# Optimization experiments

Hardware: AMD Instinct MI355X
Metric: run time of the kernel (lower is better)

## Reference

```python
import jax, jax.numpy as jnp
import numpy as np
from jax import lax

H, W = 480, 320
BS, PAD, SF, WIN = 20, 6, 4, 32        # block, zero-pad, scale, window = BS+2*PAD
NH, NW = H // BS, W // BS              # 24, 16 -> 384 blocks


def _conv(x, w, b, stride=1, pad=0):
    out = lax.conv_general_dilated(x, w, (stride, stride), [(pad, pad), (pad, pad)],
                                   dimension_numbers=('NCHW', 'OIHW', 'NCHW'))
    return out + b[None, :, None, None]


def _rep_conv(x, w, b):  # 3x3 conv with replicate padding (padding_mode='replicate')
    xp = jnp.pad(x, ((0, 0), (0, 0), (1, 1), (1, 1)), mode='edge')
    return _conv(xp, w, b)


def _maxpool2(x):
    return lax.reduce_window(x, -jnp.inf, lax.max, (1, 1, 2, 2), (1, 1, 2, 2), 'VALID')


def _pixel_shuffle(x, r=SF):  # (N, C*r*r, h, w) -> (N, C, h*r, w*r), torch ordering
    n, crr, h, w = x.shape
    c = crr // (r * r)
    return x.reshape(n, c, r, r, h, w).transpose(0, 1, 4, 2, 5, 3).reshape(n, c, h * r, w * r)


def _he(key, shape):
    std = np.sqrt(2.0 / (shape[0] * shape[2] * shape[3]))
    return jax.random.normal(key, shape, jnp.float32) * std


def setup_inputs() -> dict:
    key = jax.random.key(0)
    ks = jax.random.split(key, 16)
    return {
        'x': jax.random.normal(ks[0], (1, 3, H, W), jnp.float32),
        'cls_w1': _he(ks[1], (32, 3, 3, 3)),  'cls_b1': jnp.zeros((32,), jnp.float32),
        'cls_w2': _he(ks[2], (32, 32, 3, 3)), 'cls_b2': jnp.zeros((32,), jnp.float32),
        'cls_w3': _he(ks[3], (16, 32, 3, 3)), 'cls_b3': jnp.zeros((16,), jnp.float32),
        'cls_w4': _he(ks[4], (8, 16, 3, 3)),  'cls_b4': jnp.zeros((8,), jnp.float32),
        'cls_w5': _he(ks[5], (1, 8, 5, 5)),   'cls_b5': jnp.zeros((1,), jnp.float32),
        'lt_w1': _he(ks[6], (16, 3, 3, 3)),   'lt_b1': jnp.zeros((16,), jnp.float32),
        'lt_w2': _he(ks[7], (48, 16, 3, 3)),  'lt_b2': jnp.zeros((48,), jnp.float32),
        'cx_w1': _he(ks[8], (64, 3, 3, 3)),   'cx_b1': jnp.zeros((64,), jnp.float32),
        'cx_w2': _he(ks[9], (64, 64, 3, 3)),  'cx_b2': jnp.zeros((64,), jnp.float32),
        'cx_w3': _he(ks[10], (48, 64, 3, 3)), 'cx_b3': jnp.zeros((48,), jnp.float32),
    }


def reference(x, cls_w1, cls_b1, cls_w2, cls_b2, cls_w3, cls_b3, cls_w4, cls_b4,
              cls_w5, cls_b5, lt_w1, lt_b1, lt_w2, lt_b2,
              cx_w1, cx_b1, cx_w2, cx_b2, cx_w3, cx_b3):
    relu = jax.nn.relu
    # ---- classifier (gate) ----
    h = relu(_rep_conv(x, cls_w1, cls_b1))
    h = _maxpool2(relu(_rep_conv(h, cls_w2, cls_b2)))
    h = relu(_rep_conv(h, cls_w3, cls_b3))
    h = _maxpool2(relu(_rep_conv(h, cls_w4, cls_b4)))
    h = _conv(h, cls_w5, cls_b5, stride=BS // 4)          # (1,1,NH,NW)
    class_vector = jax.nn.sigmoid(h.reshape(-1))          # (NH*NW,)

    # ---- blockify (overlapping 32x32 windows, stride 20, zero pad 6) ----
    xp = jnp.pad(x, ((0, 0), (0, 0), (PAD, PAD), (PAD, PAD)))
    hidx = jnp.arange(NH)[:, None] * BS + jnp.arange(WIN)
    widx = jnp.arange(NW)[:, None] * BS + jnp.arange(WIN)
    t = xp[:, :, hidx]
    t = t[:, :, :, :, widx]
    blocks = t.transpose(0, 2, 4, 1, 3, 5).reshape(NH * NW, 3, WIN, WIN)

    # ---- experts (run on all blocks; mask-select == one-hot gather/scatter) ----
    lt = _pixel_shuffle(_conv(relu(_conv(blocks, lt_w1, lt_b1, pad=1)), lt_w2, lt_b2, pad=1))
    lt = jnp.clip(lt, 0.0, 1.0)
    cx = relu(_conv(blocks, cx_w1, cx_b1, pad=1))
    cx = relu(_conv(cx, cx_w2, cx_b2, pad=1))
    cx = jnp.clip(_pixel_shuffle(_conv(cx, cx_w3, cx_b3, pad=1)), 0.0, 1.0)

    is_complex = class_vector > 0.5
    out = jnp.where(is_complex[:, None, None, None], cx, lt)  # (N,3,128,128)

    # ---- crop halo and reassemble full image ----
    c0 = SF * PAD
    out = out[:, :, c0:c0 + SF * BS, c0:c0 + SF * BS]          # (N,3,80,80)
    img = out.reshape(NH, NW, 3, SF * BS, SF * BS)
    img = img.transpose(2, 0, 3, 1, 4).reshape(1, 3, NH * SF * BS, NW * SF * BS)
    return img, class_vector
```

## Files before the change

### kernel.cpp

```cpp
#include <hip/hip_runtime.h>
#include <hip/hip_bf16.h>
#include <math.h>

static constexpr int H = 480, W = 320, NH = 24, NW = 16, NB = 384;
static constexpr int HW = H * W;
static constexpr int H2 = 240, W2 = 160;
static constexpr int HW2 = H2 * W2;
static constexpr int H4 = 120, W4 = 80;
static constexpr int HW4 = H4 * W4;
static constexpr int IMG_PIX = 3 * 1920 * 1280;

typedef __attribute__((ext_vector_type(8))) short short8;
typedef __attribute__((ext_vector_type(4))) float f32x4;
typedef __attribute__((ext_vector_type(8))) unsigned short ushort8;

static constexpr int WQ_CX2 = 0;
static constexpr int WQ_CX3 = 36864;
static constexpr int WQ_LT2 = 64512;
static constexpr int WQ_FCX = 78336;
static constexpr int WQ_FLT = 80384;
static constexpr int WQ_CLS2 = 80896;
static constexpr int WPK_ALL = 108544;

__device__ __forceinline__ int iclamp(int v, int lo, int hi) {
    return v < lo ? lo : (v > hi ? hi : v);
}
__device__ __forceinline__ unsigned short f2bfu(float x) {
    __hip_bfloat16 h = __float2bfloat16(x);
    return *reinterpret_cast<unsigned short*>(&h);
}
__device__ __forceinline__ float bf2f(unsigned short u) {
    __hip_bfloat16 h = *reinterpret_cast<__hip_bfloat16*>(&u);
    return __bfloat162float(h);
}

__global__ __launch_bounds__(256) void k_prep(const float* __restrict__ x,
                                              const float* __restrict__ cls_w1,
                                              const float* __restrict__ cls_b1,
                                              const float* __restrict__ cx_w2,
                                              const float* __restrict__ cx_w3,
                                              const float* __restrict__ lt_w2,
                                              const float* __restrict__ cx_w1,
                                              const float* __restrict__ lt_w1,
                                              const float* __restrict__ cls_w2,
                                              unsigned short* __restrict__ c1s,
                                              unsigned short* __restrict__ wpk) {
    int blk = blockIdx.x;
    if (blk < 600) {
        int p = blk * 256 + threadIdx.x;
        int y = p / W, xx = p - y * W;
        float in[27];
#pragma unroll
        for (int ci = 0; ci < 3; ++ci)
#pragma unroll
            for (int dy = 0; dy < 3; ++dy) {
                int yy = iclamp(y + dy - 1, 0, H - 1);
#pragma unroll
                for (int dx = 0; dx < 3; ++dx) {
                    int xc = iclamp(xx + dx - 1, 0, W - 1);
                    in[ci * 9 + dy * 3 + dx] = x[ci * HW + yy * W + xc];
                }
            }
#pragma unroll
        for (int coc = 0; coc < 4; ++coc) {
            ushort8 hv, mv, lv;
#pragma unroll
            for (int c8 = 0; c8 < 8; ++c8) {
                int co = coc * 8 + c8;
                float acc = cls_b1[co];
#pragma unroll
                for (int k = 0; k < 27; ++k) acc = fmaf(cls_w1[co * 27 + k], in[k], acc);
                float v = fmaxf(acc, 0.f);
                unsigned short h = f2bfu(v);
                float r1 = v - bf2f(h);
                unsigned short m = f2bfu(r1);
                unsigned short l = f2bfu(r1 - bf2f(m));
                hv[c8] = h; mv[c8] = m; lv[c8] = l;
            }
            *(ushort8*)(c1s + (long)p * 32 + coc * 8) = hv;
            *(ushort8*)(c1s + (long)32 * HW + (long)p * 32 + coc * 8) = mv;
            *(ushort8*)(c1s + (long)64 * HW + (long)p * 32 + coc * 8) = lv;
        }
        return;
    }
    int i = (blk - 600) * 256 + threadIdx.x;
    if (i >= WPK_ALL) return;
    float v = 0.f;
    if (i < WQ_CX3) {
        int c = i >> 9, r = i & 511;
        int lane = r >> 3, j = r & 7;
        int col = lane & 15, kq = lane >> 4;
        int nt = c & 3, kc = (c >> 2) & 1, t = c >> 3;
        int co = nt * 16 + col, ci = kc * 32 + kq * 8 + j;
        v = cx_w2[(co * 64 + ci) * 9 + t];
    } else if (i < WQ_LT2) {
        int c = (i - WQ_CX3) >> 9, r = i & 511;
        int lane = r >> 3, j = r & 7;
        int col = lane & 15, kq = lane >> 4;
        int nt = c % 3, q = c / 3;
        int kc = q & 1, t = q >> 1;
        int co = nt * 16 + col, ci = kc * 32 + kq * 8 + j;
        v = cx_w3[(co * 64 + ci) * 9 + t];
    } else if (i < WQ_FCX) {
        int c = (i - WQ_LT2) >> 9, r = i & 511;
        int lane = r >> 3, j = r & 7;
        int col = lane & 15, kq = lane >> 4;
        int nt = c % 3, t = c / 3;
        int co = nt * 16 + col, ci = kq * 8 + j;
        v = (ci < 16) ? lt_w2[(co * 16 + ci) * 9 + t] : 0.f;
    } else if (i < WQ_FLT) {
        int c = (i - WQ_FCX) >> 9, r = i & 511;
        int lane = r >> 3, j = r & 7;
        int col = lane & 15, kq = lane >> 4;
        int co = c * 16 + col, k = kq * 8 + j;
        v = (k < 27) ? cx_w1[co * 27 + k] : 0.f;
    } else if (i < WQ_CLS2) {
        int r = i & 511;
        int lane = r >> 3, j = r & 7;
        int col = lane & 15, kq = lane >> 4;
        int k = kq * 8 + j;
        v = (k < 27) ? lt_w1[col * 27 + k] : 0.f;
    } else {
        int c = (i - WQ_CLS2) >> 9, r = i & 511;
        int lane = r >> 3, j = r & 7;
        int col = lane & 15, kq = lane >> 4;
        int nt = c & 1, q = c >> 1;
        int t = q % 9, pl = q / 9;
        int co = nt * 16 + col, ci = kq * 8 + j;
        float w = cls_w2[(co * 32 + ci) * 9 + t];
        unsigned short h = f2bfu(w);
        float r1 = w - bf2f(h);
        unsigned short m = f2bfu(r1);
        unsigned short l = f2bfu(r1 - bf2f(m));
        wpk[i] = pl == 0 ? h : (pl == 1 ? m : l);
        return;
    }
    wpk[i] = f2bfu(v);
}


template <int P>
__device__ __forceinline__ void cls2_phase(const unsigned short* __restrict__ src,
                                           unsigned short* __restrict__ sh2,
                                           const unsigned short* __restrict__ wb,
                                           f32x4 acc[4][2], int tid, int ty, int tx) {
    int lane = tid & 63, wave = tid >> 6;
    int col = lane & 15, kq = lane >> 4;
    __syncthreads();
    for (int idx = tid; idx < 1296; idx += 256) {
        int pix = idx >> 2, g = idx & 3;
        int hy = iclamp(ty * 16 + pix / 18 - 1, 0, H - 1);
        int hx = iclamp(tx * 16 + pix % 18 - 1, 0, W - 1);
        ushort8 v = *(const ushort8*)(src + ((long)(hy * W + hx)) * 32 + g * 8);
        *(ushort8*)(sh2 + pix * 32 + ((g ^ ((pix >> 1) & 3)) * 8)) = v;
    }
    __syncthreads();
#pragma unroll
    for (int t = 0; t < 9; ++t) {
        int dy = t / 3, dx = t - dy * 3;
        short8 B[2][P];
#pragma unroll
        for (int nt = 0; nt < 2; ++nt)
#pragma unroll
            for (int pl = 0; pl < P; ++pl)
                B[nt][pl] = *(const short8*)(wb + ((pl * 9 + t) * 2 + nt) * 512 + lane * 8);
#pragma unroll
        for (int i = 0; i < 4; ++i) {
            int pix = (wave * 4 + i + dy) * 18 + col + dx;
            short8 a = *(const short8*)(sh2 + pix * 32 + ((kq ^ ((pix >> 1) & 3)) * 8));
#pragma unroll
            for (int nt = 0; nt < 2; ++nt)
#pragma unroll
                for (int pl = 0; pl < P; ++pl)
                    acc[i][nt] = __builtin_amdgcn_mfma_f32_16x16x32_bf16(a, B[nt][pl],
                                                                         acc[i][nt], 0, 0, 0);
        }
    }
}

__global__ __launch_bounds__(256, 2) void k_cls2m(const unsigned short* __restrict__ c1s,
                                                  const unsigned short* __restrict__ wpk,
                                                  const float* __restrict__ b2,
                                                  float* __restrict__ c2) {
    extern __shared__ unsigned short sh2[];
    int tid = threadIdx.x;
    int tile = blockIdx.x;
    int ty = tile / 20, tx = tile - ty * 20;
    int lane = tid & 63, wave = tid >> 6;
    int col = lane & 15, kq = lane >> 4;
    const unsigned short* wb = wpk + WQ_CLS2;
    f32x4 acc[4][2];
#pragma unroll
    for (int nt = 0; nt < 2; ++nt) {
        float bv = b2[nt * 16 + col];
#pragma unroll
        for (int i = 0; i < 4; ++i) acc[i][nt] = f32x4{bv, bv, bv, bv};
    }
    cls2_phase<3>(c1s, sh2, wb, acc, tid, ty, tx);
    cls2_phase<2>(c1s + (long)32 * HW, sh2, wb + 18 * 512, acc, tid, ty, tx);
    cls2_phase<1>(c1s + (long)64 * HW, sh2, wb + 36 * 512, acc, tid, ty, tx);
    __syncthreads();
    float* pool = (float*)sh2;
#pragma unroll
    for (int i = 0; i < 4; ++i)
#pragma unroll
        for (int nt = 0; nt < 2; ++nt)
#pragma unroll
            for (int rr = 0; rr < 4; ++rr)
                pool[(nt * 16 + col) * 257 + (wave * 4 + i) * 16 + kq * 4 + rr] =
                    fmaxf(acc[i][nt][rr], 0.f);
    __syncthreads();
#pragma unroll
    for (int k = 0; k < 8; ++k) {
        int o = tid + k * 256;
        int co = o >> 6, rem = o & 63;
        int py = rem >> 3, px = rem & 7;
        const float* lp = pool + co * 257 + py * 32 + px * 2;
        float m = fmaxf(fmaxf(lp[0], lp[1]), fmaxf(lp[16], lp[17]));
        c2[co * HW2 + (ty * 8 + py) * W2 + tx * 8 + px] = m;
    }
}

__global__ __launch_bounds__(256) void k_cls3(const float* __restrict__ in,
                                              const float* __restrict__ w,
                                              const float* __restrict__ b,
                                              float* __restrict__ p3) {
    int p = blockIdx.x * 256 + threadIdx.x;
    if (p >= HW2) return;
    int cc = blockIdx.y;
    int s = blockIdx.z;
    int y = p / W2, xx = p - y * W2;
    float acc[8];
#pragma unroll
    for (int co = 0; co < 8; ++co) acc[co] = s ? 0.f : b[cc * 8 + co];
    for (int cil = 0; cil < 16; ++cil) {
        int ci = s * 16 + cil;
        float v[9];
#pragma unroll
        for (int dy = 0; dy < 3; ++dy) {
            int yy = iclamp(y + dy - 1, 0, H2 - 1);
#pragma unroll
            for (int dx = 0; dx < 3; ++dx) {
                int xc = iclamp(xx + dx - 1, 0, W2 - 1);
                v[dy * 3 + dx] = in[ci * HW2 + yy * W2 + xc];
            }
        }
#pragma unroll
        for (int co = 0; co < 8; ++co)
#pragma unroll
            for (int k = 0; k < 9; ++k)
                acc[co] = fmaf(w[(cc * 8 + co) * 288 + ci * 9 + k], v[k], acc[co]);
    }
#pragma unroll
    for (int co = 0; co < 8; ++co) p3[(s * 16 + cc * 8 + co) * HW2 + p] = acc[co];
}

__global__ __launch_bounds__(256) void k_cls4f(const float* __restrict__ p3,
                                               const float* __restrict__ w,
                                               const float* __restrict__ b,
                                               float* __restrict__ out) {
    __shared__ float lds[8 * 256];
    int t = threadIdx.x;
    int tile = blockIdx.x;
    int ty = tile / 10, tx = tile - ty * 10;
    int ly = t >> 4, lx = t & 15;
    int y = ty * 16 + ly, xx = tx * 16 + lx;
    float acc[8];
#pragma unroll
    for (int co = 0; co < 8; ++co) acc[co] = b[co];
    for (int ci = 0; ci < 16; ++ci) {
        float v[9];
#pragma unroll
        for (int dy = 0; dy < 3; ++dy) {
            int yy = iclamp(y + dy - 1, 0, H2 - 1);
#pragma unroll
            for (int dx = 0; dx < 3; ++dx) {
                int xc = iclamp(xx + dx - 1, 0, W2 - 1);
                int idx = ci * HW2 + yy * W2 + xc;
                v[dy * 3 + dx] = fmaxf(p3[idx] + p3[idx + 16 * HW2], 0.f);
            }
        }
#pragma unroll
        for (int co = 0; co < 8; ++co) {
            const float* wp = w + co * 144 + ci * 9;
#pragma unroll
            for (int k = 0; k < 9; ++k) acc[co] = fmaf(wp[k], v[k], acc[co]);
        }
    }
#pragma unroll
    for (int co = 0; co < 8; ++co) lds[co * 256 + t] = fmaxf(acc[co], 0.f);
    __syncthreads();
#pragma unroll
    for (int k = 0; k < 2; ++k) {
        int o = t + k * 256;
        int co = o >> 6, rem = o & 63;
        int py = rem >> 3, px = rem & 7;
        const float* lp = lds + co * 256 + py * 32 + px * 2;
        float m = fmaxf(fmaxf(lp[0], lp[1]), fmaxf(lp[16], lp[17]));
        out[co * HW4 + (ty * 8 + py) * W4 + tx * 8 + px] = m;
    }
}

__global__ __launch_bounds__(64) void k_cls5(const float* __restrict__ in,
                                             const float* __restrict__ w,
                                             const float* __restrict__ b,
                                             float* __restrict__ clsv,
                                             float* __restrict__ out_cls) {
    int bidx = blockIdx.x;
    int oy = bidx / NW, ox = bidx - oy * NW;
    int lane = threadIdx.x;
    float s = 0.f;
    for (int k = lane; k < 200; k += 64) {
        int ci = k / 25, r = k - ci * 25;
        int ky = r / 5, kx = r - ky * 5;
        s = fmaf(w[k], in[ci * HW4 + (oy * 5 + ky) * W4 + (ox * 5 + kx)], s);
    }
#pragma unroll
    for (int off = 32; off; off >>= 1) s += __shfl_down(s, off, 64);
    if (lane == 0) {
        float sig = 1.f / (1.f + expf(-(s + b[0])));
        clsv[bidx] = sig;
        out_cls[bidx] = sig;
    }
}

__global__ __launch_bounds__(512)
__attribute__((amdgpu_waves_per_eu(4, 8)))
void k_block(const float* __restrict__ x,
             const unsigned short* __restrict__ wpk,
             const float* __restrict__ lt_b1,
             const float* __restrict__ cx_b1,
             const float* __restrict__ lt_b2,
             const float* __restrict__ cx_b2,
             const float* __restrict__ cx_b3,
             const float* __restrict__ clsv,
             float* __restrict__ out) {
    extern __shared__ unsigned short sh[];
    unsigned short* T1 = sh;
    unsigned short* T2 = sh;
    unsigned short* XH = sh + 16384;
    unsigned short* WB = sh + 17408;
    int wg = blockIdx.x;
    int b = wg / 5, e = wg - b * 5;
    bool cx = clsv[b] > 0.5f;
    int bh = b / NW, bw = b - bh * NW;
    int base = 6 + 4 * e;
    int tid = threadIdx.x;
    int lane = tid & 63, wave = tid >> 6;
    int col = lane & 15, kq = lane >> 4;

    if (!cx) {
        ushort8 z = {0, 0, 0, 0, 0, 0, 0, 0};
        for (int i = tid; i < 1024; i += 512) *(ushort8*)(T1 + i * 8) = z;
    }
    if (tid < 340) {
        int xr = tid / 34, xcc = tid - xr * 34;
        int yg = bh * 20 + (base - 3 + xr) - 6;
        int xg = bw * 20 + (xcc - 1) - 6;
        bool ok = (unsigned)yg < (unsigned)H && (unsigned)xg < (unsigned)W;
#pragma unroll
        for (int ci = 0; ci < 3; ++ci)
            XH[ci * 340 + tid] = ok ? f2bfu(x[ci * HW + yg * W + xg])
                                    : (unsigned short)0;
    }
    __syncthreads();

    if (cx) {
        short8 Bf[4];
        float bv[4];
#pragma unroll
        for (int nt = 0; nt < 4; ++nt) {
            Bf[nt] = *(const short8*)(wpk + WQ_FCX + nt * 512 + lane * 8);
            bv[nt] = cx_b1[nt * 16 + col];
        }
#pragma unroll
        for (int i = 0; i < 2; ++i) {
            int mt = wave + 8 * i;
            int tr = mt >> 1, xc0 = (mt & 1) << 4;
            short8 av;
#pragma unroll
            for (int j = 0; j < 8; ++j) {
                int k = kq * 8 + j;
                int kk = k < 27 ? k : 0;
                int ci = kk / 9, t = kk - ci * 9;
                int dy = t / 3, dx = t - dy * 3;
                unsigned short v = XH[ci * 340 + (tr + dy) * 34 + (xc0 + col + dx)];
                av[j] = (k < 27) ? (short)v : (short)0;
            }
#pragma unroll
            for (int nt = 0; nt < 4; ++nt) {
                f32x4 acc = {bv[nt], bv[nt], bv[nt], bv[nt]};
                acc = __builtin_amdgcn_mfma_f32_16x16x32_bf16(av, Bf[nt], acc, 0, 0, 0);
                int co = nt * 16 + col;
#pragma unroll
                for (int r = 0; r < 4; ++r) {
                    int p1 = mt * 16 + kq * 4 + r;
                    T1[p1 * 64 + (((co >> 3) ^ (p1 & 7)) << 3) + (co & 7)] =
                        f2bfu(fmaxf(acc[r], 0.f));
                }
            }
        }
        {
            ushort8 nb0 = *(const ushort8*)(wpk + WQ_CX2 + tid * 8);
            *(ushort8*)(WB + tid * 8) = nb0;
        }
    } else {
        short8 Bf = *(const short8*)(wpk + WQ_FLT + lane * 8);
        float bv = lt_b1[col];
#pragma unroll
        for (int i = 0; i < 2; ++i) {
            int mt = wave + 8 * i;
            int tr = mt >> 1, xc0 = (mt & 1) << 4;
            short8 av;
#pragma unroll
            for (int j = 0; j < 8; ++j) {
                int k = kq * 8 + j;
                int kk = k < 27 ? k : 0;
                int ci = kk / 9, t = kk - ci * 9;
                int dy = t / 3, dx = t - dy * 3;
                unsigned short v = XH[ci * 340 + (tr + dy) * 34 + (xc0 + col + dx)];
                av[j] = (k < 27) ? (short)v : (short)0;
            }
            f32x4 acc = {bv, bv, bv, bv};
            acc = __builtin_amdgcn_mfma_f32_16x16x32_bf16(av, Bf, acc, 0, 0, 0);
#pragma unroll
            for (int r = 0; r < 4; ++r) {
                int p1 = mt * 16 + kq * 4 + r;
                T1[p1 * 32 + (((col >> 3) ^ ((p1 >> 1) & 3)) << 3) + (col & 7)] =
                    f2bfu(fmaxf(acc[r], 0.f));
            }
        }
        if (tid < 192) {
            ushort8 nb0 = *(const ushort8*)(wpk + WQ_LT2 + tid * 8);
            *(ushort8*)(WB + tid * 8) = nb0;
        }
    }
    __syncthreads();

    if (cx) {
        {
            f32x4 acc[2][4];
#pragma unroll
            for (int nt = 0; nt < 4; ++nt) {
                float bv = cx_b2[nt * 16 + col];
#pragma unroll
                for (int i = 0; i < 2; ++i) acc[i][nt] = f32x4{bv, bv, bv, bv};
            }
#pragma unroll
            for (int t = 0; t < 9; ++t) {
                int dy = t / 3, dx = t - dy * 3;
                ushort8 nb;
                if (t < 8)
                    nb = *(const ushort8*)(wpk + WQ_CX2 + (t + 1) * 4096 + tid * 8);
                const unsigned short* WBc = WB + (t & 1) * 4096;
                short8 B[4][2];
#pragma unroll
                for (int nt = 0; nt < 4; ++nt)
#pragma unroll
                    for (int kc = 0; kc < 2; ++kc)
                        B[nt][kc] = *(const short8*)(WBc + (kc * 4 + nt) * 512 + lane * 8);
#pragma unroll
                for (int i = 0; i < 2; ++i) {
                    int mt = wave + 8 * i;
                    if (mt >= 12) continue;
                    int tr = (mt >> 1) + dy;
                    int xs = ((mt & 1) << 4) + col + dx - 1;
                    bool xv = (unsigned)xs < 32u;
                    int xcl = xs < 0 ? 0 : (xs > 31 ? 31 : xs);
                    int p1 = tr * 32 + xcl;
#pragma unroll
                    for (int kc = 0; kc < 2; ++kc) {
                        int c = kc * 4 + kq;
                        short8 a = *(const short8*)(T1 + p1 * 64 + ((c ^ (p1 & 7)) << 3));
                        if (!xv) a = short8{0, 0, 0, 0, 0, 0, 0, 0};
#pragma unroll
                        for (int nt = 0; nt < 4; ++nt)
                            acc[i][nt] = __builtin_amdgcn_mfma_f32_16x16x32_bf16(
                                a, B[nt][kc], acc[i][nt], 0, 0, 0);
                    }
                }
                if (t < 8)
                    *(ushort8*)(WB + ((t + 1) & 1) * 4096 + tid * 8) = nb;
                __syncthreads();
            }
#pragma unroll
            for (int i = 0; i < 2; ++i) {
                int mt = wave + 8 * i;
                if (mt >= 12) continue;
#pragma unroll
                for (int nt = 0; nt < 4; ++nt) {
                    int co = nt * 16 + col;
#pragma unroll
                    for (int r = 0; r < 4; ++r) {
                        int p2 = mt * 16 + kq * 4 + r;
                        T2[p2 * 64 + (((co >> 3) ^ (p2 & 7)) << 3) + (co & 7)] =
                            f2bfu(fmaxf(acc[i][nt][r], 0.f));
                    }
                }
            }
            if (tid < 384) {
                ushort8 nb0 = *(const ushort8*)(wpk + WQ_CX3 + tid * 8);
                *(ushort8*)(WB + tid * 8) = nb0;
            }
        }
        __syncthreads();
        {
            int mt = wave;
            f32x4 acc[3];
#pragma unroll
            for (int nt = 0; nt < 3; ++nt) {
                float bv = cx_b3[nt * 16 + col];
                acc[nt] = f32x4{bv, bv, bv, bv};
            }
#pragma unroll
            for (int t = 0; t < 9; ++t) {
                int dy = t / 3, dx = t - dy * 3;
                ushort8 nb;
                if (t < 8 && tid < 384)
                    nb = *(const ushort8*)(wpk + WQ_CX3 + (t + 1) * 3072 + tid * 8);
                const unsigned short* WBc = WB + (t & 1) * 4096;
                short8 B[3][2];
#pragma unroll
                for (int nt = 0; nt < 3; ++nt)
#pragma unroll
                    for (int kc = 0; kc < 2; ++kc)
                        B[nt][kc] = *(const short8*)(WBc + (kc * 3 + nt) * 512 + lane * 8);
                int tr2 = (mt >> 1) + dy;
                int xs = ((mt & 1) << 4) + col + dx - 1;
                bool xv = (unsigned)xs < 32u;
                int xcl = xs < 0 ? 0 : (xs > 31 ? 31 : xs);
                int p2 = tr2 * 32 + xcl;
#pragma unroll
                for (int kc = 0; kc < 2; ++kc) {
                    int c = kc * 4 + kq;
                    short8 a = *(const short8*)(T2 + p2 * 64 + ((c ^ (p2 & 7)) << 3));
                    if (!xv) a = short8{0, 0, 0, 0, 0, 0, 0, 0};
#pragma unroll
                    for (int nt = 0; nt < 3; ++nt)
                        acc[nt] = __builtin_amdgcn_mfma_f32_16x16x32_bf16(
                            a, B[nt][kc], acc[nt], 0, 0, 0);
                }
                if (t < 8) {
                    if (tid < 384)
                        *(ushort8*)(WB + ((t + 1) & 1) * 4096 + tid * 8) = nb;
                    __syncthreads();
                }
            }
            int py = base + (mt >> 1);
#pragma unroll
            for (int nt = 0; nt < 3; ++nt) {
                int co = nt * 16 + col;
                int ch = co >> 4, dy2 = (co >> 2) & 3, dx2 = co & 3;
#pragma unroll
                for (int r = 0; r < 4; ++r) {
                    int p = mt * 16 + kq * 4 + r;
                    int px = p & 31;
                    int s0 = px * 4 + dx2 - 24;
                    if ((unsigned)s0 < 80u) {
                        int r0 = py * 4 + dy2 - 24;
                        float v = fminf(fmaxf(acc[nt][r], 0.f), 1.f);
                        out[ch * 2457600 + (bh * 80 + r0) * 1280 + bw * 80 + s0] = v;
                    }
                }
            }
        }
    } else {
        int mt = wave;
        f32x4 acc[3];
#pragma unroll
        for (int nt = 0; nt < 3; ++nt) {
            float bv = lt_b2[nt * 16 + col];
            acc[nt] = f32x4{bv, bv, bv, bv};
        }
#pragma unroll
        for (int t = 0; t < 9; ++t) {
            int dy = t / 3, dx = t - dy * 3;
            ushort8 nb;
            if (t < 8 && tid < 192)
                nb = *(const ushort8*)(wpk + WQ_LT2 + (t + 1) * 1536 + tid * 8);
            const unsigned short* WBc = WB + (t & 1) * 4096;
            short8 B[3];
#pragma unroll
            for (int nt = 0; nt < 3; ++nt)
                B[nt] = *(const short8*)(WBc + nt * 512 + lane * 8);
            int tr = (mt >> 1) + 1 + dy;
            int xs = ((mt & 1) << 4) + col + dx - 1;
            bool xv = (unsigned)xs < 32u;
            int xcl = xs < 0 ? 0 : (xs > 31 ? 31 : xs);
            int p1 = tr * 32 + xcl;
            short8 a = *(const short8*)(T1 + p1 * 32 + ((kq ^ ((p1 >> 1) & 3)) << 3));
            if (!xv) a = short8{0, 0, 0, 0, 0, 0, 0, 0};
#pragma unroll
            for (int nt = 0; nt < 3; ++nt)
                acc[nt] = __builtin_amdgcn_mfma_f32_16x16x32_bf16(a, B[nt], acc[nt], 0, 0, 0);
            if (t < 8) {
                if (tid < 192)
                    *(ushort8*)(WB + ((t + 1) & 1) * 4096 + tid * 8) = nb;
                __syncthreads();
            }
        }
        int py = base + (mt >> 1);
#pragma unroll
        for (int nt = 0; nt < 3; ++nt) {
            int co = nt * 16 + col;
            int ch = co >> 4, dy2 = (co >> 2) & 3, dx2 = co & 3;
#pragma unroll
            for (int r = 0; r < 4; ++r) {
                int p = mt * 16 + kq * 4 + r;
                int px = p & 31;
                int s0 = px * 4 + dx2 - 24;
                if ((unsigned)s0 < 80u) {
                    int r0 = py * 4 + dy2 - 24;
                    float v = fminf(fmaxf(acc[nt][r], 0.f), 1.f);
                    out[ch * 2457600 + (bh * 80 + r0) * 1280 + bw * 80 + s0] = v;
                }
            }
        }
    }
}

extern "C" void kernel_launch(void* const* d_in, const int* in_sizes, int n_in,
                              void* d_out, int out_size, void* d_ws, size_t ws_size,
                              hipStream_t stream) {
    const float* x      = (const float*)d_in[0];
    const float* cls_w1 = (const float*)d_in[1];
    const float* cls_b1 = (const float*)d_in[2];
    const float* cls_w2 = (const float*)d_in[3];
    const float* cls_b2 = (const float*)d_in[4];
    const float* cls_w3 = (const float*)d_in[5];
    const float* cls_b3 = (const float*)d_in[6];
    const float* cls_w4 = (const float*)d_in[7];
    const float* cls_b4 = (const float*)d_in[8];
    const float* cls_w5 = (const float*)d_in[9];
    const float* cls_b5 = (const float*)d_in[10];
    const float* lt_w1  = (const float*)d_in[11];
    const float* lt_b1  = (const float*)d_in[12];
    const float* lt_w2  = (const float*)d_in[13];
    const float* lt_b2  = (const float*)d_in[14];
    const float* cx_w1  = (const float*)d_in[15];
    const float* cx_b1  = (const float*)d_in[16];
    const float* cx_w2  = (const float*)d_in[17];
    const float* cx_b2  = (const float*)d_in[18];
    const float* cx_w3  = (const float*)d_in[19];
    const float* cx_b3  = (const float*)d_in[20];

    float* ws = (float*)d_ws;
    float* out = (float*)d_out;

    size_t off = 0;
    float* c2 = ws + off;   off += (size_t)32 * HW2;
    float* c4 = ws + off;   off += (size_t)8 * HW4;
    float* clsv = ws + off; off += 384;
    unsigned short* wpk = (unsigned short*)(ws + off); off += (WPK_ALL + 1) / 2;
    size_t fixed = off;

    unsigned short* c1s = (unsigned short*)(ws + fixed);
    float* p3 = ws + fixed + (size_t)48 * HW;

    (void)hipFuncSetAttribute((const void*)k_cls2m,
                              hipFuncAttributeMaxDynamicSharedMemorySize, 32896);
    (void)hipFuncSetAttribute((const void*)k_block,
                              hipFuncAttributeMaxDynamicSharedMemorySize, 51200);

    k_prep<<<600 + (WPK_ALL + 255) / 256, 256, 0, stream>>>(
        x, cls_w1, cls_b1, cx_w2, cx_w3, lt_w2, cx_w1, lt_w1, cls_w2, c1s, wpk);
    k_cls2m<<<600, 256, 32896, stream>>>(c1s, wpk, cls_b2, c2);
    k_cls3<<<dim3(150, 2, 2), 256, 0, stream>>>(c2, cls_w3, cls_b3, p3);
    k_cls4f<<<150, 256, 0, stream>>>(p3, cls_w4, cls_b4, c4);
    k_cls5<<<NB, 64, 0, stream>>>(c4, cls_w5, cls_b5, clsv, out + IMG_PIX);
    k_block<<<NB * 5, 512, 51200, stream>>>(x, wpk, lt_b1, cx_b1, lt_b2, cx_b2,
                                            cx_b3, clsv, out);
}
```

Measured before the change: 154.9 us.

## Fuse cls conv3 and conv4 into one tiled kernel with LDS halo

Merges the third and fourth classifier convolutions into a single kernel. Each 16x16 tile computes conv3 outputs for an 18x18 halo region into shared memory, then runs conv4 and the 2x2 maxpool from that buffer. This removes the p3 intermediate round-trip through global memory and one kernel launch. In exchange the halo pixels are recomputed, and only 150 blocks do all 32-input-channel work, with a 324-position loop that leaves threads idle on its second pass, so parallelism drops compared to the 600-block split version.

```diff
diff --git a/kernel.cpp b/kernel.cpp
--- a/kernel.cpp
+++ b/kernel.cpp
@@ -221,83 +221,74 @@
     }
 }
 
-__global__ __launch_bounds__(256) void k_cls3(const float* __restrict__ in,
-                                              const float* __restrict__ w,
-                                              const float* __restrict__ b,
-                                              float* __restrict__ p3) {
-    int p = blockIdx.x * 256 + threadIdx.x;
-    if (p >= HW2) return;
-    int cc = blockIdx.y;
-    int s = blockIdx.z;
-    int y = p / W2, xx = p - y * W2;
-    float acc[8];
-#pragma unroll
-    for (int co = 0; co < 8; ++co) acc[co] = s ? 0.f : b[cc * 8 + co];
-    for (int cil = 0; cil < 16; ++cil) {
-        int ci = s * 16 + cil;
-        float v[9];
-#pragma unroll
-        for (int dy = 0; dy < 3; ++dy) {
-            int yy = iclamp(y + dy - 1, 0, H2 - 1);
-#pragma unroll
-            for (int dx = 0; dx < 3; ++dx) {
-                int xc = iclamp(xx + dx - 1, 0, W2 - 1);
-                v[dy * 3 + dx] = in[ci * HW2 + yy * W2 + xc];
-            }
-        }
-#pragma unroll
-        for (int co = 0; co < 8; ++co)
-#pragma unroll
-            for (int k = 0; k < 9; ++k)
-                acc[co] = fmaf(w[(cc * 8 + co) * 288 + ci * 9 + k], v[k], acc[co]);
-    }
-#pragma unroll
-    for (int co = 0; co < 8; ++co) p3[(s * 16 + cc * 8 + co) * HW2 + p] = acc[co];
-}
-
-__global__ __launch_bounds__(256) void k_cls4f(const float* __restrict__ p3,
-                                               const float* __restrict__ w,
-                                               const float* __restrict__ b,
-                                               float* __restrict__ out) {
-    __shared__ float lds[8 * 256];
+__global__ __launch_bounds__(256) void k_cls34(const float* __restrict__ c2,
+                                               const float* __restrict__ w3,
+                                               const float* __restrict__ b3,
+                                               const float* __restrict__ w4,
+                                               const float* __restrict__ b4,
+                                               float* __restrict__ c4out) {
+    __shared__ float c3t[16 * 324];
     int t = threadIdx.x;
     int tile = blockIdx.x;
     int ty = tile / 10, tx = tile - ty * 10;
+    for (int pos = t; pos < 324; pos += 256) {
+        int hy = iclamp(ty * 16 + pos / 18 - 1, 0, H2 - 1);
+        int hx = iclamp(tx * 16 + pos % 18 - 1, 0, W2 - 1);
+        float acc[16];
+#pragma unroll
+        for (int co = 0; co < 16; ++co) acc[co] = b3[co];
+        for (int ci = 0; ci < 32; ++ci) {
+            float v[9];
+#pragma unroll
+            for (int dy = 0; dy < 3; ++dy) {
+                int yy = iclamp(hy + dy - 1, 0, H2 - 1);
+#pragma unroll
+                for (int dx = 0; dx < 3; ++dx) {
+                    int xc = iclamp(hx + dx - 1, 0, W2 - 1);
+                    v[dy * 3 + dx] = c2[ci * HW2 + yy * W2 + xc];
+                }
+            }
+#pragma unroll
+            for (int co = 0; co < 16; ++co)
+#pragma unroll
+                for (int k = 0; k < 9; ++k)
+                    acc[co] = fmaf(w3[co * 288 + ci * 9 + k], v[k], acc[co]);
+        }
+#pragma unroll
+        for (int co = 0; co < 16; ++co) c3t[co * 324 + pos] = fmaxf(acc[co], 0.f);
+    }
+    __syncthreads();
     int ly = t >> 4, lx = t & 15;
-    int y = ty * 16 + ly, xx = tx * 16 + lx;
-    float acc[8];
-#pragma unroll
-    for (int co = 0; co < 8; ++co) acc[co] = b[co];
+    float acc4[8];
+#pragma unroll
+    for (int co = 0; co < 8; ++co) acc4[co] = b4[co];
     for (int ci = 0; ci < 16; ++ci) {
         float v[9];
 #pragma unroll
-        for (int dy = 0; dy < 3; ++dy) {
-            int yy = iclamp(y + dy - 1, 0, H2 - 1);
-#pragma unroll
-            for (int dx = 0; dx < 3; ++dx) {
-                int xc = iclamp(xx + dx - 1, 0, W2 - 1);
-                int idx = ci * HW2 + yy * W2 + xc;
-                v[dy * 3 + dx] = fmaxf(p3[idx] + p3[idx + 16 * HW2], 0.f);
-            }
-        }
+        for (int dy = 0; dy < 3; ++dy)
+#pragma unroll
+            for (int dx = 0; dx < 3; ++dx)
+                v[dy * 3 + dx] = c3t[ci * 324 + (ly + dy) * 18 + (lx + dx)];
 #pragma unroll
         for (int co = 0; co < 8; ++co) {
-            const float* wp = w + co * 144 + ci * 9;
-#pragma unroll
-            for (int k = 0; k < 9; ++k) acc[co] = fmaf(wp[k], v[k], acc[co]);
-        }
-    }
-#pragma unroll
-    for (int co = 0; co < 8; ++co) lds[co * 256 + t] = fmaxf(acc[co], 0.f);
+            const float* wp = w4 + co * 144 + ci * 9;
+#pragma unroll
+            for (int k = 0; k < 9; ++k) acc4[co] = fmaf(wp[k], v[k], acc4[co]);
+        }
+    }
+    __syncthreads();
+    float* pool = c3t;
+#pragma unroll
+    for (int co = 0; co < 8; ++co) pool[co * 256 + t] = fmaxf(acc4[co], 0.f);
     __syncthreads();
 #pragma unroll
     for (int k = 0; k < 2; ++k) {
         int o = t + k * 256;
         int co = o >> 6, rem = o & 63;
         int py = rem >> 3, px = rem & 7;
-        const float* lp = lds + co * 256 + py * 32 + px * 2;
+        const float* lp = pool + co * 256 + py * 32 + px * 2;
         float m = fmaxf(fmaxf(lp[0], lp[1]), fmaxf(lp[16], lp[17]));
-        out[co * HW4 + (ty * 8 + py) * W4 + tx * 8 + px] = m;
+        c4out[co * HW4 + (ty * 8 + py) * W4 + tx * 8 + px] = m;
     }
 }
 
@@ -655,7 +646,6 @@
     size_t fixed = off;
 
     unsigned short* c1s = (unsigned short*)(ws + fixed);
-    float* p3 = ws + fixed + (size_t)48 * HW;
 
     (void)hipFuncSetAttribute((const void*)k_cls2m,
                               hipFuncAttributeMaxDynamicSharedMemorySize, 32896);
@@ -665,8 +655,7 @@
     k_prep<<<600 + (WPK_ALL + 255) / 256, 256, 0, stream>>>(
         x, cls_w1, cls_b1, cx_w2, cx_w3, lt_w2, cx_w1, lt_w1, cls_w2, c1s, wpk);
     k_cls2m<<<600, 256, 32896, stream>>>(c1s, wpk, cls_b2, c2);
-    k_cls3<<<dim3(150, 2, 2), 256, 0, stream>>>(c2, cls_w3, cls_b3, p3);
-    k_cls4f<<<150, 256, 0, stream>>>(p3, cls_w4, cls_b4, c4);
+    k_cls34<<<150, 256, 0, stream>>>(c2, cls_w3, cls_b3, cls_w4, cls_b4, c4);
     k_cls5<<<NB, 64, 0, stream>>>(c4, cls_w5, cls_b5, clsv, out + IMG_PIX);
     k_block<<<NB * 5, 512, 51200, stream>>>(x, wpk, lt_b1, cx_b1, lt_b2, cx_b2,
                                             cx_b3, clsv, out);
```

Result: slower. 211.6 us (+36.6%).
